# Kernel optimization log

Measured on AMD Instinct MI355X. Metric: run time of the kernel, lower is better.

Reference implementation:

```python
import jax, jax.numpy as jnp
import numpy as np


def setup_inputs() -> dict:
    key = jax.random.key(0)
    k1, k2 = jax.random.split(key)
    B, N, M, D = 8, 4096, 4096, 3
    return {
        "input": jax.random.normal(k1, (B, N, D), dtype=jnp.float32),
        "target": jax.random.normal(k2, (B, M, D), dtype=jnp.float32),
    }


def reference(input, target):
    x2 = jnp.sum(input * input, axis=-1)          # [B, N]
    y2 = jnp.sum(target * target, axis=-1)        # [B, M]
    xy = jnp.einsum("bnd,bmd->bnm", input, target)  # [B, N, M]
    sqdist = x2[:, :, None] + y2[:, None, :] - 2.0 * xy
    sqdist = jnp.maximum(sqdist, 0.0)  # clamp numerical negatives
    sqdist1 = jnp.min(sqdist, axis=2)  # nearest target for each input point [B, N]
    sqdist2 = jnp.min(sqdist, axis=1)  # nearest input for each target point [B, M]
    return jnp.mean(sqdist1) + jnp.mean(sqdist2)
```

## Files before the change

### kernel.cpp

```cpp
#include <hip/hip_runtime.h>
#include <math.h>

#define BATCH  8
#define NPTS   4096
#define TPB    256
#define QPT    4
#define QCHUNK (TPB * QPT)
#define NQC    (NPTS / QCHUNK)
#define NCC    16
#define CTILE  (NPTS / NCC)

__global__ __launch_bounds__(TPB) void chamfer_min_kernel(
    const float* __restrict__ input,
    const float* __restrict__ target,
    unsigned int* __restrict__ best)
{
    const int dir = blockIdx.z;
    const int b   = blockIdx.y;
    const int qc  = blockIdx.x & (NQC - 1);
    const int cc  = blockIdx.x >> 2;

    const float* __restrict__ qp = (dir ? target : input) + (size_t)b * NPTS * 3;
    const float* __restrict__ cp = (dir ? input  : target) + (size_t)b * NPTS * 3;

    __shared__ float4 cand[CTILE];
    {
        const int c = cc * CTILE + threadIdx.x;
        const float cx = cp[3 * c + 0];
        const float cy = cp[3 * c + 1];
        const float cz = cp[3 * c + 2];
        cand[threadIdx.x] = make_float4(-2.0f * cx, -2.0f * cy, -2.0f * cz,
                                        fmaf(cx, cx, fmaf(cy, cy, cz * cz)));
    }

    const int q0 = qc * QCHUNK + (int)threadIdx.x * QPT;
    float px[QPT], py[QPT], pz[QPT], pmin[QPT];
    #pragma unroll
    for (int k = 0; k < QPT; ++k) {
        px[k] = qp[3 * (q0 + k) + 0];
        py[k] = qp[3 * (q0 + k) + 1];
        pz[k] = qp[3 * (q0 + k) + 2];
        pmin[k] = 3.4e38f;
    }
    __syncthreads();

    #pragma unroll 4
    for (int m = 0; m < CTILE; ++m) {
        const float4 c = cand[m];
        #pragma unroll
        for (int k = 0; k < QPT; ++k) {
            const float t = fmaf(px[k], c.x,
                            fmaf(py[k], c.y,
                            fmaf(pz[k], c.z, c.w)));
            pmin[k] = fminf(pmin[k], t);
        }
    }

    unsigned int* bq = best + ((size_t)(dir * BATCH + b)) * NPTS + q0;
    #pragma unroll
    for (int k = 0; k < QPT; ++k) {
        const float x2 = fmaf(px[k], px[k], fmaf(py[k], py[k], pz[k] * pz[k]));
        const float v  = fmaxf(pmin[k] + x2, 0.0f);
        atomicMin(&bq[k], __float_as_uint(v));
    }
}

__global__ __launch_bounds__(TPB) void chamfer_reduce_kernel(
    const unsigned int* __restrict__ best, float* __restrict__ out)
{
    const int i = (blockIdx.x * TPB + (int)threadIdx.x) * 4;
    const uint4 u = *(const uint4*)(best + i);
    float s = __uint_as_float(u.x) + __uint_as_float(u.y) +
              __uint_as_float(u.z) + __uint_as_float(u.w);
    #pragma unroll
    for (int off = 32; off > 0; off >>= 1)
        s += __shfl_down(s, off, 64);

    __shared__ float wsum[TPB / 64];
    if ((threadIdx.x & 63) == 0) wsum[threadIdx.x >> 6] = s;
    __syncthreads();
    if (threadIdx.x == 0) {
        const float t = wsum[0] + wsum[1] + wsum[2] + wsum[3];
        atomicAdd(out, t * (1.0f / (float)(BATCH * NPTS)));
    }
}

extern "C" void kernel_launch(void* const* d_in, const int* in_sizes, int n_in,
                              void* d_out, int out_size, void* d_ws, size_t ws_size,
                              hipStream_t stream) {
    const float* input  = (const float*)d_in[0];
    const float* target = (const float*)d_in[1];
    float* out = (float*)d_out;
    unsigned int* best = (unsigned int*)d_ws;

    hipMemsetAsync(best, 0x7F, (size_t)2 * BATCH * NPTS * sizeof(unsigned int), stream);
    hipMemsetAsync(out, 0, sizeof(float), stream);

    dim3 grid1(NQC * NCC, BATCH, 2);
    chamfer_min_kernel<<<grid1, dim3(TPB), 0, stream>>>(input, target, best);

    dim3 grid2((2 * BATCH * NPTS) / (TPB * 4));
    chamfer_reduce_kernel<<<grid2, dim3(TPB), 0, stream>>>(best, out);
}
```

Before: 83.63 us.

## Write per-chunk partial minima instead of atomics, raise queries per thread

```diff
diff --git a/kernel.cpp b/kernel.cpp
--- a/kernel.cpp
+++ b/kernel.cpp
@@ -4,27 +4,28 @@
 #define BATCH  8
 #define NPTS   4096
 #define TPB    256
-#define QPT    4
+#define QPT    8
 #define QCHUNK (TPB * QPT)
 #define NQC    (NPTS / QCHUNK)
-#define NCC    16
+#define NCC    32
 #define CTILE  (NPTS / NCC)
+#define NQTOT  (2 * BATCH * NPTS)
 
 __global__ __launch_bounds__(TPB) void chamfer_min_kernel(
     const float* __restrict__ input,
     const float* __restrict__ target,
-    unsigned int* __restrict__ best)
+    float* __restrict__ partial)
 {
     const int dir = blockIdx.z;
     const int b   = blockIdx.y;
     const int qc  = blockIdx.x & (NQC - 1);
-    const int cc  = blockIdx.x >> 2;
+    const int cc  = blockIdx.x >> 1;
 
     const float* __restrict__ qp = (dir ? target : input) + (size_t)b * NPTS * 3;
     const float* __restrict__ cp = (dir ? input  : target) + (size_t)b * NPTS * 3;
 
     __shared__ float4 cand[CTILE];
-    {
+    if (threadIdx.x < CTILE) {
         const int c = cc * CTILE + threadIdx.x;
         const float cx = cp[3 * c + 0];
         const float cy = cp[3 * c + 1];
@@ -34,44 +35,57 @@
     }
 
     const int q0 = qc * QCHUNK + (int)threadIdx.x * QPT;
-    float px[QPT], py[QPT], pz[QPT], pmin[QPT];
+    float qv[3 * QPT];
+    {
+        const float4* qp4 = (const float4*)(qp + 3 * q0);
+        #pragma unroll
+        for (int j = 0; j < 6; ++j) {
+            const float4 v = qp4[j];
+            qv[4 * j + 0] = v.x; qv[4 * j + 1] = v.y;
+            qv[4 * j + 2] = v.z; qv[4 * j + 3] = v.w;
+        }
+    }
+    float pmin[QPT];
     #pragma unroll
-    for (int k = 0; k < QPT; ++k) {
-        px[k] = qp[3 * (q0 + k) + 0];
-        py[k] = qp[3 * (q0 + k) + 1];
-        pz[k] = qp[3 * (q0 + k) + 2];
-        pmin[k] = 3.4e38f;
-    }
+    for (int k = 0; k < QPT; ++k) pmin[k] = 3.4e38f;
     __syncthreads();
 
-    #pragma unroll 4
+    #pragma unroll 2
     for (int m = 0; m < CTILE; ++m) {
         const float4 c = cand[m];
         #pragma unroll
         for (int k = 0; k < QPT; ++k) {
-            const float t = fmaf(px[k], c.x,
-                            fmaf(py[k], c.y,
-                            fmaf(pz[k], c.z, c.w)));
+            const float t = fmaf(qv[3 * k + 0], c.x,
+                            fmaf(qv[3 * k + 1], c.y,
+                            fmaf(qv[3 * k + 2], c.z, c.w)));
             pmin[k] = fminf(pmin[k], t);
         }
     }
 
-    unsigned int* bq = best + ((size_t)(dir * BATCH + b)) * NPTS + q0;
+    float res[QPT];
     #pragma unroll
     for (int k = 0; k < QPT; ++k) {
-        const float x2 = fmaf(px[k], px[k], fmaf(py[k], py[k], pz[k] * pz[k]));
-        const float v  = fmaxf(pmin[k] + x2, 0.0f);
-        atomicMin(&bq[k], __float_as_uint(v));
+        const float x2 = fmaf(qv[3 * k + 0], qv[3 * k + 0],
+                         fmaf(qv[3 * k + 1], qv[3 * k + 1],
+                              qv[3 * k + 2] * qv[3 * k + 2]));
+        res[k] = fmaxf(pmin[k] + x2, 0.0f);
     }
+    float4* pout = (float4*)(partial + (size_t)cc * NQTOT +
+                             ((size_t)(dir * BATCH + b)) * NPTS + q0);
+    pout[0] = make_float4(res[0], res[1], res[2], res[3]);
+    pout[1] = make_float4(res[4], res[5], res[6], res[7]);
 }
 
 __global__ __launch_bounds__(TPB) void chamfer_reduce_kernel(
-    const unsigned int* __restrict__ best, float* __restrict__ out)
+    const float* __restrict__ partial, float* __restrict__ out)
 {
-    const int i = (blockIdx.x * TPB + (int)threadIdx.x) * 4;
-    const uint4 u = *(const uint4*)(best + i);
-    float s = __uint_as_float(u.x) + __uint_as_float(u.y) +
-              __uint_as_float(u.z) + __uint_as_float(u.w);
+    const int g = blockIdx.x * TPB + (int)threadIdx.x;
+    float v = partial[g];
+    #pragma unroll
+    for (int cc = 1; cc < NCC; ++cc)
+        v = fminf(v, partial[(size_t)cc * NQTOT + g]);
+
+    float s = v;
     #pragma unroll
     for (int off = 32; off > 0; off >>= 1)
         s += __shfl_down(s, off, 64);
@@ -91,14 +105,12 @@
     const float* input  = (const float*)d_in[0];
     const float* target = (const float*)d_in[1];
     float* out = (float*)d_out;
-    unsigned int* best = (unsigned int*)d_ws;
+    float* partial = (float*)d_ws;
 
-    hipMemsetAsync(best, 0x7F, (size_t)2 * BATCH * NPTS * sizeof(unsigned int), stream);
     hipMemsetAsync(out, 0, sizeof(float), stream);
 
     dim3 grid1(NQC * NCC, BATCH, 2);
-    chamfer_min_kernel<<<grid1, dim3(TPB), 0, stream>>>(input, target, best);
+    chamfer_min_kernel<<<grid1, dim3(TPB), 0, stream>>>(input, target, partial);
 
-    dim3 grid2((2 * BATCH * NPTS) / (TPB * 4));
-    chamfer_reduce_kernel<<<grid2, dim3(TPB), 0, stream>>>(best, out);
+    chamfer_reduce_kernel<<<dim3(NQTOT / TPB), dim3(TPB), 0, stream>>>(partial, out);
 }
```

Measured after the change: 85.28 us. Within noise of the previous version (+2.0%).
